# Kernel tuning notes

Hardware: AMD Instinct MI355X
Metric: run time of the kernel (lower is better)

The kernel has to match this reference:

```python
import jax, jax.numpy as jnp
import numpy as np

EPS = 1e-12  # TF l2_normalize epsilon


def setup_inputs() -> dict:
    key = jax.random.key(0)
    k1, k2 = jax.random.split(key)
    B, V, F = 32, 200000, 400000
    vertices = jax.random.normal(k1, (B, V, 3), dtype=jnp.float32)
    faces = jax.random.randint(k2, (F, 3), 0, V, dtype=jnp.int32)
    return {"vertices": vertices, "faces": faces}


def reference(vertices, faces):
    # vertices: [B, V, 3], faces: [F, 3]
    # Gather triangle vertices: [B, F, 3(verts), 3(xyz)]
    tri = vertices[:, faces, :]
    v0, v1, v2 = tri[..., 0, :], tri[..., 1, :], tri[..., 2, :]
    e1 = v0 - v1
    e2 = v2 - v1
    face_normals = jnp.cross(e2, e1)  # [B, F, 3], unnormalized
    # Scatter-add face normals onto each of the 3 face vertices
    vertex_normals = jnp.zeros_like(vertices)
    for i in range(3):
        vertex_normals = vertex_normals.at[:, faces[:, i], :].add(face_normals)
    # l2 normalize (TF semantics: x * rsqrt(max(sum(x^2), eps)))
    sq = jnp.sum(vertex_normals * vertex_normals, axis=-1, keepdims=True)
    vertex_normals = vertex_normals * jax.lax.rsqrt(jnp.maximum(sq, EPS))
    return vertex_normals
```

## Files before the change

### kernel.cpp

```cpp
#include <hip/hip_runtime.h>

#define EPS 1e-12f
#define CAP 32
#define CAPU 8

typedef unsigned long long ull;


__global__ void zero_ints(int* __restrict__ p, int n) {
    int i = blockIdx.x * blockDim.x + threadIdx.x;
    if (i < n) p[i] = 0;
}

__global__ __launch_bounds__(1024) void transpose_in(const float* __restrict__ verts,
                                                     float4* __restrict__ verts4T,
                                                     int V) {
    __shared__ float sx[32][33], sy[32][33], sz[32][33];
    int tx = threadIdx.x & 31, ty = threadIdx.x >> 5;
    int v0 = blockIdx.x * 32;
    const float* p = verts + ((size_t)ty * V + (v0 + tx)) * 3;
    float x = __builtin_nontemporal_load(p + 0);
    float y = __builtin_nontemporal_load(p + 1);
    float z = __builtin_nontemporal_load(p + 2);
    sx[ty][tx] = x; sy[ty][tx] = y; sz[ty][tx] = z;
    __syncthreads();
    verts4T[(size_t)(v0 + ty) * 32 + tx] =
        make_float4(sx[tx][ty], sy[tx][ty], sz[tx][ty], 0.f);
}

__global__ void fill_corner(const int* __restrict__ faces, int* __restrict__ cursor,
                            ull* __restrict__ ell, int E) {
    int t = blockIdx.x * blockDim.x + threadIdx.x;
    if (t >= E) return;
    int f = t / 3;
    int c = t - 3 * f;
    int base = 3 * f;
    int iv = faces[base + c];
    int ia = faces[base + (c == 2 ? 0 : c + 1)];
    int ib = faces[base + (c == 0 ? 2 : c - 1)];
    int s = atomicAdd(&cursor[iv], 1);
    if (s < CAP) {
        ull e = ((ull)(unsigned)ib << 32) | (unsigned)ia;
        __builtin_nontemporal_store(e, ell + (size_t)iv * CAP + s);
    }
}

__global__ __launch_bounds__(1024) void gather_t(const float4* __restrict__ verts4T,
                                                 const int* __restrict__ deg,
                                                 const ull* __restrict__ ell,
                                                 float* __restrict__ out,
                                                 int V) {
    __shared__ float sx[32][33], sy[32][33], sz[32][33];
    int b = threadIdx.x & 31;
    int vi = threadIdx.x >> 5;
    int v = blockIdx.x * 32 + vi;

    int d = min(deg[v], CAP);
    float4 c = verts4T[(size_t)v * 32 + b];
    const ull* ev = ell + (size_t)v * CAP;
    ull e[CAPU];
#pragma unroll
    for (int s = 0; s < CAPU; s++)
        e[s] = ev[s];
    __builtin_amdgcn_sched_barrier(0);

    float4 A[CAPU], Bq[CAPU];
#pragma unroll
    for (int s = 0; s < CAPU; s++) {
        unsigned ia = (s < d) ? (unsigned)(e[s] & 0xffffffffull) : 0u;
        unsigned ib = (s < d) ? (unsigned)(e[s] >> 32) : 0u;
        A[s]  = verts4T[(size_t)ia * 32 + b];
        Bq[s] = verts4T[(size_t)ib * 32 + b];
    }
    __builtin_amdgcn_sched_barrier(0);

    float vx = c.x, vy = c.y, vz = c.z;
    float ax = 0.f, ay = 0.f, az = 0.f;
#pragma unroll
    for (int s = 0; s < CAPU; s++) {
        if (s < d) {
            float aX = A[s].x - vx, aY = A[s].y - vy, aZ = A[s].z - vz;
            float bX = Bq[s].x - vx, bY = Bq[s].y - vy, bZ = Bq[s].z - vz;
            ax += aY * bZ - aZ * bY;
            ay += aZ * bX - aX * bZ;
            az += aX * bY - aY * bX;
        }
    }
    for (int s = CAPU; s < d; s++) {
        ull cu = ev[s];
        float4 Av = verts4T[(size_t)(unsigned)(cu & 0xffffffffull) * 32 + b];
        float4 Bv = verts4T[(size_t)(unsigned)(cu >> 32) * 32 + b];
        float aX = Av.x - vx, aY = Av.y - vy, aZ = Av.z - vz;
        float bX = Bv.x - vx, bY = Bv.y - vy, bZ = Bv.z - vz;
        ax += aY * bZ - aZ * bY;
        ay += aZ * bX - aX * bZ;
        az += aX * bY - aY * bX;
    }

    float scn = rsqrtf(fmaxf(ax * ax + ay * ay + az * az, EPS));
    sx[vi][b] = ax * scn; sy[vi][b] = ay * scn; sz[vi][b] = az * scn;
    __syncthreads();

    float* o = out + ((size_t)vi * V + (size_t)blockIdx.x * 32 + b) * 3;
    __builtin_nontemporal_store(sx[b][vi], o + 0);
    __builtin_nontemporal_store(sy[b][vi], o + 1);
    __builtin_nontemporal_store(sz[b][vi], o + 2);
}

extern "C" void kernel_launch(void* const* d_in, const int* in_sizes, int n_in,
                              void* d_out, int out_size, void* d_ws, size_t ws_size,
                              hipStream_t stream) {
    const float* verts = (const float*)d_in[0];
    const int* faces = (const int*)d_in[1];
    float* out = (float*)d_out;

    const int V = 200000;
    const int F = in_sizes[1] / 3;
    const int B = in_sizes[0] / (3 * V);
    const int E = 3 * F;
    (void)B;

    char* w = (char*)d_ws;
    float4* verts4T = (float4*)w; w += (size_t)V * 32 * sizeof(float4);
    int* cursor = (int*)w;        w += (size_t)V * sizeof(int);
    ull* ell = (ull*)w;

    zero_ints<<<(V + 255) / 256, 256, 0, stream>>>(cursor, V);
    transpose_in<<<V / 32, 1024, 0, stream>>>(verts, verts4T, V);
    fill_corner<<<(E + 255) / 256, 256, 0, stream>>>(faces, cursor, ell, E);
    gather_t<<<V / 32, 1024, 0, stream>>>(verts4T, cursor, ell, out, V);
}
```

Before: 434.0 us.

## Fuse transpose and adjacency fill into one launch; use SoA 96-float vertex rows

Merges the vertex transpose and the corner-list fill into one kernel, split by block index, so both independent prep stages run concurrently in a single launch. Also replaces the padded float4-per-batch layout with an SoA row of 96 floats per vertex (x, y, z each as 32 contiguous batch values). This drops the padding lane, cutting gathered bytes by a quarter, at the cost of three scalar loads instead of one vector load per neighbor. The fill part now runs with 1024-thread blocks instead of 256.

```diff
diff --git a/kernel.cpp b/kernel.cpp
--- a/kernel.cpp
+++ b/kernel.cpp
@@ -12,40 +12,44 @@
     if (i < n) p[i] = 0;
 }
 
-__global__ __launch_bounds__(1024) void transpose_in(const float* __restrict__ verts,
-                                                     float4* __restrict__ verts4T,
-                                                     int V) {
-    __shared__ float sx[32][33], sy[32][33], sz[32][33];
-    int tx = threadIdx.x & 31, ty = threadIdx.x >> 5;
-    int v0 = blockIdx.x * 32;
-    const float* p = verts + ((size_t)ty * V + (v0 + tx)) * 3;
-    float x = __builtin_nontemporal_load(p + 0);
-    float y = __builtin_nontemporal_load(p + 1);
-    float z = __builtin_nontemporal_load(p + 2);
-    sx[ty][tx] = x; sy[ty][tx] = y; sz[ty][tx] = z;
-    __syncthreads();
-    verts4T[(size_t)(v0 + ty) * 32 + tx] =
-        make_float4(sx[tx][ty], sy[tx][ty], sz[tx][ty], 0.f);
-}
-
-__global__ void fill_corner(const int* __restrict__ faces, int* __restrict__ cursor,
-                            ull* __restrict__ ell, int E) {
-    int t = blockIdx.x * blockDim.x + threadIdx.x;
-    if (t >= E) return;
-    int f = t / 3;
-    int c = t - 3 * f;
-    int base = 3 * f;
-    int iv = faces[base + c];
-    int ia = faces[base + (c == 2 ? 0 : c + 1)];
-    int ib = faces[base + (c == 0 ? 2 : c - 1)];
-    int s = atomicAdd(&cursor[iv], 1);
-    if (s < CAP) {
-        ull e = ((ull)(unsigned)ib << 32) | (unsigned)ia;
-        __builtin_nontemporal_store(e, ell + (size_t)iv * CAP + s);
+__global__ __launch_bounds__(1024) void prep_kernel(const float* __restrict__ verts,
+                                                    float* __restrict__ vT,
+                                                    const int* __restrict__ faces,
+                                                    int* __restrict__ cursor,
+                                                    ull* __restrict__ ell,
+                                                    int V, int tblk, int E) {
+    if ((int)blockIdx.x < tblk) {
+        __shared__ float sx[32][33], sy[32][33], sz[32][33];
+        int tx = threadIdx.x & 31, ty = threadIdx.x >> 5;
+        int v0 = blockIdx.x * 32;
+        const float* p = verts + ((size_t)ty * V + (v0 + tx)) * 3;
+        float x = __builtin_nontemporal_load(p + 0);
+        float y = __builtin_nontemporal_load(p + 1);
+        float z = __builtin_nontemporal_load(p + 2);
+        sx[ty][tx] = x; sy[ty][tx] = y; sz[ty][tx] = z;
+        __syncthreads();
+        float* o = vT + (size_t)(v0 + ty) * 96;
+        o[tx]      = sx[tx][ty];
+        o[32 + tx] = sy[tx][ty];
+        o[64 + tx] = sz[tx][ty];
+    } else {
+        int t = (blockIdx.x - tblk) * 1024 + threadIdx.x;
+        if (t >= E) return;
+        int f = t / 3;
+        int c = t - 3 * f;
+        int base = 3 * f;
+        int iv = faces[base + c];
+        int ia = faces[base + (c == 2 ? 0 : c + 1)];
+        int ib = faces[base + (c == 0 ? 2 : c - 1)];
+        int s = atomicAdd(&cursor[iv], 1);
+        if (s < CAP) {
+            ull e = ((ull)(unsigned)ib << 32) | (unsigned)ia;
+            __builtin_nontemporal_store(e, ell + (size_t)iv * CAP + s);
+        }
     }
 }
 
-__global__ __launch_bounds__(1024) void gather_t(const float4* __restrict__ verts4T,
+__global__ __launch_bounds__(1024) void gather_t(const float* __restrict__ vT,
                                                  const int* __restrict__ deg,
                                                  const ull* __restrict__ ell,
                                                  float* __restrict__ out,
@@ -56,7 +60,8 @@
     int v = blockIdx.x * 32 + vi;
 
     int d = min(deg[v], CAP);
-    float4 c = verts4T[(size_t)v * 32 + b];
+    const float* crow = vT + (size_t)v * 96;
+    float vx = crow[b], vy = crow[32 + b], vz = crow[64 + b];
     const ull* ev = ell + (size_t)v * CAP;
     ull e[CAPU];
 #pragma unroll
@@ -64,23 +69,24 @@
         e[s] = ev[s];
     __builtin_amdgcn_sched_barrier(0);
 
-    float4 A[CAPU], Bq[CAPU];
+    float Ax[CAPU], Ay[CAPU], Az[CAPU], Bx[CAPU], By[CAPU], Bz[CAPU];
 #pragma unroll
     for (int s = 0; s < CAPU; s++) {
         unsigned ia = (s < d) ? (unsigned)(e[s] & 0xffffffffull) : 0u;
         unsigned ib = (s < d) ? (unsigned)(e[s] >> 32) : 0u;
-        A[s]  = verts4T[(size_t)ia * 32 + b];
-        Bq[s] = verts4T[(size_t)ib * 32 + b];
+        const float* ra = vT + (size_t)ia * 96;
+        const float* rb = vT + (size_t)ib * 96;
+        Ax[s] = ra[b]; Ay[s] = ra[32 + b]; Az[s] = ra[64 + b];
+        Bx[s] = rb[b]; By[s] = rb[32 + b]; Bz[s] = rb[64 + b];
     }
     __builtin_amdgcn_sched_barrier(0);
 
-    float vx = c.x, vy = c.y, vz = c.z;
     float ax = 0.f, ay = 0.f, az = 0.f;
 #pragma unroll
     for (int s = 0; s < CAPU; s++) {
         if (s < d) {
-            float aX = A[s].x - vx, aY = A[s].y - vy, aZ = A[s].z - vz;
-            float bX = Bq[s].x - vx, bY = Bq[s].y - vy, bZ = Bq[s].z - vz;
+            float aX = Ax[s] - vx, aY = Ay[s] - vy, aZ = Az[s] - vz;
+            float bX = Bx[s] - vx, bY = By[s] - vy, bZ = Bz[s] - vz;
             ax += aY * bZ - aZ * bY;
             ay += aZ * bX - aX * bZ;
             az += aX * bY - aY * bX;
@@ -88,10 +94,10 @@
     }
     for (int s = CAPU; s < d; s++) {
         ull cu = ev[s];
-        float4 Av = verts4T[(size_t)(unsigned)(cu & 0xffffffffull) * 32 + b];
-        float4 Bv = verts4T[(size_t)(unsigned)(cu >> 32) * 32 + b];
-        float aX = Av.x - vx, aY = Av.y - vy, aZ = Av.z - vz;
-        float bX = Bv.x - vx, bY = Bv.y - vy, bZ = Bv.z - vz;
+        const float* ra = vT + (size_t)(unsigned)(cu & 0xffffffffull) * 96;
+        const float* rb = vT + (size_t)(unsigned)(cu >> 32) * 96;
+        float aX = ra[b] - vx, aY = ra[32 + b] - vy, aZ = ra[64 + b] - vz;
+        float bX = rb[b] - vx, bY = rb[32 + b] - vy, bZ = rb[64 + b] - vz;
         ax += aY * bZ - aZ * bY;
         ay += aZ * bX - aX * bZ;
         az += aX * bY - aY * bX;
@@ -121,12 +127,16 @@
     (void)B;
 
     char* w = (char*)d_ws;
-    float4* verts4T = (float4*)w; w += (size_t)V * 32 * sizeof(float4);
-    int* cursor = (int*)w;        w += (size_t)V * sizeof(int);
+    float* vT = (float*)w;  w += (size_t)V * 96 * sizeof(float);
+    int* cursor = (int*)w;  w += (size_t)V * sizeof(int);
     ull* ell = (ull*)w;
 
     zero_ints<<<(V + 255) / 256, 256, 0, stream>>>(cursor, V);
-    transpose_in<<<V / 32, 1024, 0, stream>>>(verts, verts4T, V);
-    fill_corner<<<(E + 255) / 256, 256, 0, stream>>>(faces, cursor, ell, E);
-    gather_t<<<V / 32, 1024, 0, stream>>>(verts4T, cursor, ell, out, V);
+
+    int tblk = V / 32;
+    int fblk = (E + 1023) / 1024;
+    prep_kernel<<<tblk + fblk, 1024, 0, stream>>>(verts, vT, faces, cursor, ell,
+                                                  V, tblk, E);
+
+    gather_t<<<V / 32, 1024, 0, stream>>>(vT, cursor, ell, out, V);
 }
```

Result: faster. 398.6 us (-8.2%).
